# Optimization experiments

Hardware: AMD Instinct MI355X
Metric: run time of the kernel (lower is better)

## Reference

```python
import jax, jax.numpy as jnp
import numpy as np

M = 8192   # predicted boxes
N = 8192   # ground-truth boxes
W_CENTER, W_SIZE, W_IOU = 1.0, 0.5, 2.0
MATCH_THRESH = 5.0


def setup_inputs() -> dict:
    key = jax.random.key(0)
    k1, k2, k3, k4 = jax.random.split(key, 4)
    centers = jax.random.uniform(k1, (N, 3), dtype=jnp.float32) * 100.0
    sizes = jax.random.uniform(k2, (N, 3), dtype=jnp.float32) * 3.0 + 1.0
    yaw = jax.random.uniform(k3, (N, 1), dtype=jnp.float32) * (2.0 * jnp.pi) - jnp.pi
    gt_boxes = jnp.concatenate([centers, sizes, yaw], axis=1)  # [N,7]
    # preds = perturbed gts so the 5.0 m matching gate actually fires
    pred_boxes = gt_boxes + 0.5 * jax.random.normal(k4, (M, 7), dtype=jnp.float32)
    return {"pred_boxes": pred_boxes, "gt_boxes": gt_boxes}


def _greedy_match(pred_boxes, gt_boxes):
    """Sequential greedy nearest-center matching (torch loop -> lax.scan).
    Column deletion in the original is equivalent to masking with an
    availability vector: argmin over remaining columns with first-tie wins.
    Returns (mask [M] bool: pred i matched, idx [M] int: matched gt index)."""
    # [M,N] center distance matrix (the memory-heavy irregular part)
    diff = pred_boxes[:, None, :3] - gt_boxes[None, :, :3]
    dist = jnp.sqrt(jnp.sum(diff * diff, axis=-1))

    def step(avail, d_row):
        dm = jnp.where(avail, d_row, jnp.inf)
        j = jnp.argmin(dm)
        ok = dm[j] < MATCH_THRESH
        avail = avail.at[j].set(jnp.logical_and(avail[j], jnp.logical_not(ok)))
        return avail, (ok, j)

    avail0 = jnp.ones((gt_boxes.shape[0],), dtype=bool)
    _, (mask, idx) = jax.lax.scan(step, avail0, dist)
    return mask, idx


def _smooth_l1(x):
    a = jnp.abs(x)
    return jnp.where(a < 1.0, 0.5 * a * a, a - 0.5)


def _iou_2d(b1, b2):
    # axis-aligned BEV IoU using (x, y, l, w)
    x1, y1, l1, w1 = b1[:, 0], b1[:, 1], b1[:, 3], b1[:, 4]
    x2, y2, l2, w2 = b2[:, 0], b2[:, 1], b2[:, 3], b2[:, 4]
    iw = jnp.clip(jnp.minimum(x1 + l1 / 2, x2 + l2 / 2) - jnp.maximum(x1 - l1 / 2, x2 - l2 / 2), 0.0)
    ih = jnp.clip(jnp.minimum(y1 + w1 / 2, y2 + w2 / 2) - jnp.maximum(y1 - w1 / 2, y2 - w2 / 2), 0.0)
    inter = iw * ih
    union = l1 * w1 + l2 * w2 - inter
    return inter / (union + 1e-6)


def _loss(pred_boxes, gt_boxes, mask, idx):
    mg = gt_boxes[idx]                              # [M,7] matched gts
    m = mask.astype(pred_boxes.dtype)               # [M]
    k = jnp.maximum(jnp.sum(m), 1.0)                # number of matches
    loss_center = jnp.sum(m[:, None] * _smooth_l1(pred_boxes[:, :3] - mg[:, :3])) / (3.0 * k)
    loss_size = jnp.sum(m[:, None] * _smooth_l1(pred_boxes[:, 3:6] - mg[:, 3:6])) / (3.0 * k)
    d = pred_boxes[:, 6] - mg[:, 6]
    d = jnp.arctan2(jnp.sin(d), jnp.cos(d))         # wrap to (-pi, pi]
    loss_orient = jnp.sum(m * _smooth_l1(d)) / k
    loss_iou = jnp.sum(m * (1.0 - _iou_2d(pred_boxes, mg))) / k
    return W_CENTER * loss_center + W_SIZE * (loss_size + loss_orient) + W_IOU * loss_iou


def reference(pred_boxes, gt_boxes):
    mask, idx = _greedy_match(pred_boxes, gt_boxes)
    return _loss(pred_boxes, gt_boxes, mask, idx)
```

## Files before the change

### kernel.cpp

```cpp
#include <hip/hip_runtime.h>
#include <stdint.h>

#define MROWS 8192
#define NGT   8192
#define KC    8
#define KL    2
#define RPL   4
#define THRESH2_BITS 0x41C7FFFFu

__device__ __forceinline__ unsigned dist2_bits(float px, float py, float pz,
                                               float gx, float gy, float gz) {
#pragma clang fp contract(off)
  float dx = px - gx;
  float dy = py - gy;
  float dz = pz - gz;
  float s = (dx * dx + dy * dy) + dz * dz;
  return __float_as_uint(s);
}

__device__ __forceinline__ unsigned long long wave_min64(unsigned long long v) {
#pragma unroll
  for (int off = 32; off >= 1; off >>= 1) {
    unsigned long long o = __shfl_xor(v, off, 64);
    v = (o < v) ? o : v;
  }
  return v;
}

template <int K>
__device__ __forceinline__ void insert_sorted(unsigned (&kd)[K], unsigned (&ki)[K],
                                              unsigned key, unsigned j) {
#pragma unroll
  for (int t = K - 1; t >= 1; --t) {
    bool a = key < kd[t];
    bool b = key < kd[t - 1];
    if (a) {
      if (b) { kd[t] = kd[t - 1]; ki[t] = ki[t - 1]; }
      else   { kd[t] = key;       ki[t] = j; }
    }
  }
  if (key < kd[0]) { kd[0] = key; ki[0] = j; }
}

template <int K>
__device__ __forceinline__ void extract8(unsigned (&kd)[K], unsigned (&ki)[K], int lane,
                                         unsigned& resd, unsigned& resi,
                                         unsigned long long& e8) {
#pragma unroll
  for (int rr = 0; rr < KC; ++rr) {
    unsigned long long head = ((unsigned long long)kd[0] << 32) | (unsigned long long)ki[0];
    unsigned long long m = wave_min64(head);
    if (head == m) {
#pragma unroll
      for (int t = 0; t < K - 1; ++t) { kd[t] = kd[t + 1]; ki[t] = ki[t + 1]; }
      kd[K - 1] = 0xFFFFFFFFu; ki[K - 1] = 0xFFFFFFFFu;
    }
    if (lane == rr) { resd = (unsigned)(m >> 32); resi = (unsigned)m; }
    e8 = m;
  }
}

__global__ __launch_bounds__(256) void pack_kernel(const float* __restrict__ gt,
                                                   float4* __restrict__ cen) {
  int j = blockIdx.x * 256 + threadIdx.x;
  if (j < NGT) cen[j] = make_float4(gt[j * 7 + 0], gt[j * 7 + 1], gt[j * 7 + 2], 0.0f);
}

__global__ __launch_bounds__(256, 8) void topk_kernel(const float* __restrict__ pred,
                                                      const float4* __restrict__ cen,
                                                      unsigned* __restrict__ cand) {
  const int tid = threadIdx.x;
  const int lane = tid & 63;
  const int row = (blockIdx.x * 256 + tid) >> 6;

  float px = pred[(size_t)row * 7 + 0];
  float py = pred[(size_t)row * 7 + 1];
  float pz = pred[(size_t)row * 7 + 2];

  unsigned kd[KL], ki[KL];
#pragma unroll
  for (int t = 0; t < KL; ++t) { kd[t] = 0xFFFFFFFFu; ki[t] = 0xFFFFFFFFu; }

#pragma unroll 2
  for (int j0 = 0; j0 < NGT / 64; ++j0) {
    int j = j0 * 64 + lane;
    float4 c = cen[j];
    unsigned key = dist2_bits(px, py, pz, c.x, c.y, c.z);
    if (key < kd[KL - 1]) insert_sorted<KL>(kd, ki, key, (unsigned)j);
  }

  unsigned long long guard =
      ((unsigned long long)kd[KL - 1] << 32) | (unsigned long long)ki[KL - 1];
  unsigned resd = 0, resi = 0;
  unsigned long long e8 = 0;
  extract8<KL>(kd, ki, lane, resd, resi, e8);

  if (__ballot(guard < e8) != 0ull) {
    unsigned fd[KC], fi[KC];
#pragma unroll
    for (int t = 0; t < KC; ++t) { fd[t] = 0xFFFFFFFFu; fi[t] = 0xFFFFFFFFu; }
    for (int j0 = 0; j0 < NGT / 64; ++j0) {
      int j = j0 * 64 + lane;
      float4 c = cen[j];
      unsigned key = dist2_bits(px, py, pz, c.x, c.y, c.z);
      if (key < fd[KC - 1]) insert_sorted<KC>(fd, fi, key, (unsigned)j);
    }
    unsigned long long dummy;
    extract8<KC>(fd, fi, lane, resd, resi, dummy);
  }
  if (lane < KC)
    cand[(size_t)row * KC + lane] = (resi << 1) | (resd < THRESH2_BITS ? 1u : 0u);
}

__global__ __launch_bounds__(64) void greedy_kernel(const unsigned* __restrict__ cand,
                                                    const float* __restrict__ pred,
                                                    const float4* __restrict__ cen,
                                                    unsigned* __restrict__ match) {
  __shared__ unsigned avail[NGT / 32];
  __shared__ unsigned claim[NGT];
  const int lane = threadIdx.x;

  for (int w = lane; w < NGT / 32; w += 64) avail[w] = 0xFFFFFFFFu;
  for (int j = lane; j < NGT; j += 64) claim[j] = 0xFFFFFFFFu;
  __syncthreads();

  unsigned ci_[RPL][KC], ni_[RPL][KC];
  bool first = true;

  for (int base = 0; base < MROWS; base += 64 * RPL) {
    const int nAct = 64 * RPL;

    if (first) {
#pragma unroll
      for (int q = 0; q < RPL; ++q) {
        const uint4* cr = (const uint4*)(cand + (size_t)(base + lane + 64 * q) * KC);
        uint4 a = cr[0], b = cr[1];
        ci_[q][0] = a.x; ci_[q][1] = a.y; ci_[q][2] = a.z; ci_[q][3] = a.w;
        ci_[q][4] = b.x; ci_[q][5] = b.y; ci_[q][6] = b.z; ci_[q][7] = b.w;
      }
      first = false;
    } else {
#pragma unroll
      for (int q = 0; q < RPL; ++q)
#pragma unroll
        for (int t = 0; t < KC; ++t) ci_[q][t] = ni_[q][t];
    }
#pragma unroll
    for (int q = 0; q < RPL; ++q) {
      int pr = base + nAct + lane + 64 * q;
      if (pr >= MROWS) pr = MROWS - 1;
      const uint4* cr = (const uint4*)(cand + (size_t)pr * KC);
      uint4 a = cr[0], b = cr[1];
      ni_[q][0] = a.x; ni_[q][1] = a.y; ni_[q][2] = a.z; ni_[q][3] = a.w;
      ni_[q][4] = b.x; ni_[q][5] = b.y; ni_[q][6] = b.z; ni_[q][7] = b.w;
    }

    unsigned m[RPL];
#pragma unroll
    for (int q = 0; q < RPL; ++q) {
      unsigned mm = 0;
#pragma unroll
      for (int t = 0; t < KC; ++t) {
        unsigned g = ci_[q][t] >> 1;
        mm |= ((avail[g >> 5] >> (g & 31)) & 1u) << t;
      }
      m[q] = mm;
    }

    int floor_ = 0;
    unsigned pe[RPL];
    bool cl[RPL];
    int rounds = 0;

    while (true) {
      while (true) {
#pragma unroll
        for (int q = 0; q < RPL; ++q) {
          int o = lane + 64 * q;
          unsigned e = 0;
#pragma unroll
          for (int t = KC - 1; t >= 0; --t)
            if (m[q] & (1u << t)) e = ci_[q][t];
          pe[q] = e;
          cl[q] = (o >= floor_) && (m[q] != 0u) && (e & 1u);
        }
#pragma unroll
        for (int q = 0; q < RPL; ++q)
          if (cl[q]) atomicMin(&claim[pe[q] >> 1], (unsigned)(lane + 64 * q));
        __builtin_amdgcn_wave_barrier();
        bool any = false;
        bool lost[RPL];
#pragma unroll
        for (int q = 0; q < RPL; ++q) {
          lost[q] = cl[q] && (claim[pe[q] >> 1] < (unsigned)(lane + 64 * q));
          any |= lost[q];
        }
        if (__ballot(any) == 0ull) break;
#pragma unroll
        for (int q = 0; q < RPL; ++q)
          if (lost[q]) m[q] &= (m[q] - 1u);
        if (++rounds > 2100) {
#pragma unroll
          for (int q = 0; q < RPL; ++q)
            if (lane + 64 * q >= floor_) m[q] = 0u;
        }
      }

      unsigned fe = 0xFFFFu;
#pragma unroll
      for (int q = 0; q < RPL; ++q) {
        unsigned o = (unsigned)(lane + 64 * q);
        if (o >= (unsigned)floor_ && m[q] == 0u && o < fe) fe = o;
      }
#pragma unroll
      for (int off = 32; off >= 1; off >>= 1) {
        unsigned o2 = __shfl_xor(fe, off, 64);
        fe = o2 < fe ? o2 : fe;
      }
      int feI = (fe == 0xFFFFu) ? nAct : (int)fe;

#pragma unroll
      for (int q = 0; q < RPL; ++q) {
        int o = lane + 64 * q;
        if (o >= floor_ && o < feI) {
          unsigned g = pe[q] >> 1;
          match[base + o] = (cl[q] ? 0x80000000u : 0u) | g;
          if (cl[q]) atomicAnd(&avail[g >> 5], ~(1u << (g & 31)));
        }
      }
      __builtin_amdgcn_wave_barrier();
      if (feI == nAct) break;

      {
        const int r = base + feI;
        float fx = pred[(size_t)r * 7 + 0];
        float fy = pred[(size_t)r * 7 + 1];
        float fz = pred[(size_t)r * 7 + 2];
        unsigned long long best = ~0ull;
        for (int j0 = 0; j0 < NGT / 64; ++j0) {
          int j = j0 * 64 + lane;
          if ((avail[j >> 5] >> (j & 31)) & 1u) {
            float4 c = cen[j];
            unsigned sb = dist2_bits(fx, fy, fz, c.x, c.y, c.z);
            unsigned long long key = ((unsigned long long)sb << 32) | (unsigned)j;
            if (key < best) best = key;
          }
        }
        unsigned long long mm2 = wave_min64(best);
        unsigned gstar = 0xFFFFFFFFu;
        if (mm2 != ~0ull) {
          unsigned sb = (unsigned)(mm2 >> 32);
          unsigned j = (unsigned)mm2;
          bool ok = sb < THRESH2_BITS;
          if (lane == 0) {
            match[r] = (ok ? 0x80000000u : 0u) | j;
            if (ok) atomicAnd(&avail[j >> 5], ~(1u << (j & 31)));
          }
          if (ok) gstar = j;
        } else if (lane == 0) {
          match[r] = 0u;
        }
        __builtin_amdgcn_wave_barrier();
        if (gstar != 0xFFFFFFFFu) {
#pragma unroll
          for (int q = 0; q < RPL; ++q)
#pragma unroll
            for (int t = 0; t < KC; ++t)
              if ((ci_[q][t] >> 1) == gstar) m[q] &= ~(1u << t);
        }
        floor_ = feI + 1;
        if (floor_ >= nAct) break;
      }
    }

#pragma unroll
    for (int q = 0; q < RPL; ++q)
#pragma unroll
      for (int t = 0; t < KC; ++t) claim[ci_[q][t] >> 1] = 0xFFFFFFFFu;
    __builtin_amdgcn_wave_barrier();
  }
}

__device__ __forceinline__ float smooth_l1(float x) {
  float a = fabsf(x);
  return (a < 1.0f) ? (0.5f * a * a) : (a - 0.5f);
}

__global__ __launch_bounds__(256) void loss_kernel(const float* __restrict__ pred,
                                                   const float* __restrict__ gt,
                                                   const unsigned* __restrict__ match,
                                                   float* __restrict__ acc) {
  int i = blockIdx.x * 256 + threadIdx.x;
  float vc = 0.f, vs = 0.f, vo = 0.f, vi = 0.f, vk = 0.f;
  if (i < MROWS) {
    unsigned r = match[i];
    if (r & 0x80000000u) {
      unsigned j = r & 0x7FFFFFFFu;
      float p[7], g[7];
#pragma unroll
      for (int t = 0; t < 7; ++t) { p[t] = pred[i * 7 + t]; g[t] = gt[j * 7 + t]; }
      vc = smooth_l1(p[0] - g[0]) + smooth_l1(p[1] - g[1]) + smooth_l1(p[2] - g[2]);
      vs = smooth_l1(p[3] - g[3]) + smooth_l1(p[4] - g[4]) + smooth_l1(p[5] - g[5]);
      float d = p[6] - g[6];
      float w = d - 6.283185307179586f * rintf(d * 0.15915494309189535f);
      vo = smooth_l1(w);
      float iw = fminf(p[0] + p[3] * 0.5f, g[0] + g[3] * 0.5f) -
                 fmaxf(p[0] - p[3] * 0.5f, g[0] - g[3] * 0.5f);
      iw = fmaxf(iw, 0.0f);
      float ih = fminf(p[1] + p[4] * 0.5f, g[1] + g[4] * 0.5f) -
                 fmaxf(p[1] - p[4] * 0.5f, g[1] - g[4] * 0.5f);
      ih = fmaxf(ih, 0.0f);
      float inter = iw * ih;
      float uni = p[3] * p[4] + g[3] * g[4] - inter;
      vi = 1.0f - inter / (uni + 1e-6f);
      vk = 1.0f;
    }
  }
#pragma unroll
  for (int off = 32; off >= 1; off >>= 1) {
    vc += __shfl_down(vc, off, 64);
    vs += __shfl_down(vs, off, 64);
    vo += __shfl_down(vo, off, 64);
    vi += __shfl_down(vi, off, 64);
    vk += __shfl_down(vk, off, 64);
  }
  if ((threadIdx.x & 63) == 0) {
    atomicAdd(&acc[0], vc);
    atomicAdd(&acc[1], vs);
    atomicAdd(&acc[2], vo);
    atomicAdd(&acc[3], vi);
    atomicAdd(&acc[4], vk);
  }
}

__global__ void finalize_kernel(const float* __restrict__ acc, float* __restrict__ out) {
  float k = fmaxf(acc[4], 1.0f);
  float loss = acc[0] / (3.0f * k)
             + 0.5f * (acc[1] / (3.0f * k) + acc[2] / k)
             + 2.0f * (acc[3] / k);
  out[0] = loss;
}

extern "C" void kernel_launch(void* const* d_in, const int* in_sizes, int n_in,
                              void* d_out, int out_size, void* d_ws, size_t ws_size,
                              hipStream_t stream) {
  const float* pred = (const float*)d_in[0];
  const float* gt   = (const float*)d_in[1];
  char* ws = (char*)d_ws;
  float* acc       = (float*)ws;
  unsigned* match  = (unsigned*)(ws + 1024);
  unsigned* cand   = (unsigned*)(ws + 33792);
  float4* cen      = (float4*)(ws + 295936);

  hipMemsetAsync(acc, 0, 32, stream);
  pack_kernel<<<NGT / 256, 256, 0, stream>>>(gt, cen);
  topk_kernel<<<MROWS / 4, 256, 0, stream>>>(pred, cen, cand);
  greedy_kernel<<<1, 64, 0, stream>>>(cand, pred, cen, match);
  loss_kernel<<<MROWS / 256, 256, 0, stream>>>(pred, gt, match, acc);
  finalize_kernel<<<1, 1, 0, stream>>>(acc, (float*)d_out);
}
```

Baseline: 258.1 us.

## Tile GT centers through shared memory, two rows per wave; fold finalize into loss

The top-k distance kernel now stages GT centers through a double-buffered shared-memory tile and has each wave process two prediction rows. Each loaded center is reused across rows, which halves global/L2 traffic per row and the number of blocks. The finalize kernel is removed: the last loss block, found with an atomic ticket counter, computes the output, saving one launch. The trade-offs are added block barriers, more registers (launch bounds relaxed to 4), and fewer waves in flight.

```diff
diff --git a/kernel.cpp b/kernel.cpp
--- a/kernel.cpp
+++ b/kernel.cpp
@@ -5,6 +5,7 @@
 #define NGT   8192
 #define KC    8
 #define KL    2
+#define RPW   2
 #define RPL   4
 #define THRESH2_BITS 0x41C7FFFFu
 
@@ -66,50 +67,78 @@
   if (j < NGT) cen[j] = make_float4(gt[j * 7 + 0], gt[j * 7 + 1], gt[j * 7 + 2], 0.0f);
 }
 
-__global__ __launch_bounds__(256, 8) void topk_kernel(const float* __restrict__ pred,
+__global__ __launch_bounds__(256, 4) void topk_kernel(const float* __restrict__ pred,
                                                       const float4* __restrict__ cen,
                                                       unsigned* __restrict__ cand) {
+  __shared__ float4 tile[2][256];
   const int tid = threadIdx.x;
   const int lane = tid & 63;
-  const int row = (blockIdx.x * 256 + tid) >> 6;
-
-  float px = pred[(size_t)row * 7 + 0];
-  float py = pred[(size_t)row * 7 + 1];
-  float pz = pred[(size_t)row * 7 + 2];
-
-  unsigned kd[KL], ki[KL];
-#pragma unroll
-  for (int t = 0; t < KL; ++t) { kd[t] = 0xFFFFFFFFu; ki[t] = 0xFFFFFFFFu; }
-
-#pragma unroll 2
-  for (int j0 = 0; j0 < NGT / 64; ++j0) {
-    int j = j0 * 64 + lane;
-    float4 c = cen[j];
-    unsigned key = dist2_bits(px, py, pz, c.x, c.y, c.z);
-    if (key < kd[KL - 1]) insert_sorted<KL>(kd, ki, key, (unsigned)j);
-  }
-
-  unsigned long long guard =
-      ((unsigned long long)kd[KL - 1] << 32) | (unsigned long long)ki[KL - 1];
-  unsigned resd = 0, resi = 0;
-  unsigned long long e8 = 0;
-  extract8<KL>(kd, ki, lane, resd, resi, e8);
-
-  if (__ballot(guard < e8) != 0ull) {
-    unsigned fd[KC], fi[KC];
-#pragma unroll
-    for (int t = 0; t < KC; ++t) { fd[t] = 0xFFFFFFFFu; fi[t] = 0xFFFFFFFFu; }
-    for (int j0 = 0; j0 < NGT / 64; ++j0) {
-      int j = j0 * 64 + lane;
-      float4 c = cen[j];
-      unsigned key = dist2_bits(px, py, pz, c.x, c.y, c.z);
-      if (key < fd[KC - 1]) insert_sorted<KC>(fd, fi, key, (unsigned)j);
-    }
-    unsigned long long dummy;
-    extract8<KC>(fd, fi, lane, resd, resi, dummy);
-  }
-  if (lane < KC)
-    cand[(size_t)row * KC + lane] = (resi << 1) | (resd < THRESH2_BITS ? 1u : 0u);
+  const int wave = (blockIdx.x * 256 + tid) >> 6;
+  const int r0 = wave * RPW;
+
+  float px[RPW], py[RPW], pz[RPW];
+#pragma unroll
+  for (int r = 0; r < RPW; ++r) {
+    px[r] = pred[(size_t)(r0 + r) * 7 + 0];
+    py[r] = pred[(size_t)(r0 + r) * 7 + 1];
+    pz[r] = pred[(size_t)(r0 + r) * 7 + 2];
+  }
+
+  unsigned kd[RPW][KL], ki[RPW][KL];
+#pragma unroll
+  for (int r = 0; r < RPW; ++r)
+#pragma unroll
+    for (int t = 0; t < KL; ++t) { kd[r][t] = 0xFFFFFFFFu; ki[r][t] = 0xFFFFFFFFu; }
+
+  tile[0][tid] = cen[tid];
+  __syncthreads();
+
+  for (int t = 0; t < NGT / 256; ++t) {
+    float4 nreg;
+    if (t < NGT / 256 - 1) nreg = cen[(t + 1) * 256 + tid];
+
+#pragma unroll
+    for (int i = 0; i < 4; ++i) {
+      float4 c = tile[t & 1][i * 64 + lane];
+      int j = t * 256 + i * 64 + lane;
+#pragma unroll
+      for (int r = 0; r < RPW; ++r) {
+        unsigned key = dist2_bits(px[r], py[r], pz[r], c.x, c.y, c.z);
+        if (key < kd[r][KL - 1]) insert_sorted<KL>(kd[r], ki[r], key, (unsigned)j);
+      }
+    }
+    __syncthreads();
+    if (t < NGT / 256 - 1) {
+      tile[(t + 1) & 1][tid] = nreg;
+      __syncthreads();
+    }
+  }
+
+#pragma unroll
+  for (int r = 0; r < RPW; ++r) {
+    const int row = r0 + r;
+    unsigned long long guard =
+        ((unsigned long long)kd[r][KL - 1] << 32) | (unsigned long long)ki[r][KL - 1];
+    unsigned resd = 0, resi = 0;
+    unsigned long long e8 = 0;
+    extract8<KL>(kd[r], ki[r], lane, resd, resi, e8);
+
+    if (__ballot(guard < e8) != 0ull) {
+      unsigned fd[KC], fi[KC];
+#pragma unroll
+      for (int t = 0; t < KC; ++t) { fd[t] = 0xFFFFFFFFu; fi[t] = 0xFFFFFFFFu; }
+      for (int j0 = 0; j0 < NGT / 64; ++j0) {
+        int j = j0 * 64 + lane;
+        float4 c = cen[j];
+        unsigned key = dist2_bits(px[r], py[r], pz[r], c.x, c.y, c.z);
+        if (key < fd[KC - 1]) insert_sorted<KC>(fd, fi, key, (unsigned)j);
+      }
+      unsigned long long dummy;
+      extract8<KC>(fd, fi, lane, resd, resi, dummy);
+    }
+    if (lane < KC)
+      cand[(size_t)row * KC + lane] = (resi << 1) | (resd < THRESH2_BITS ? 1u : 0u);
+  }
 }
 
 __global__ __launch_bounds__(64) void greedy_kernel(const unsigned* __restrict__ cand,
@@ -289,7 +318,8 @@
 __global__ __launch_bounds__(256) void loss_kernel(const float* __restrict__ pred,
                                                    const float* __restrict__ gt,
                                                    const unsigned* __restrict__ match,
-                                                   float* __restrict__ acc) {
+                                                   float* __restrict__ acc,
+                                                   float* __restrict__ out) {
   int i = blockIdx.x * 256 + threadIdx.x;
   float vc = 0.f, vs = 0.f, vo = 0.f, vi = 0.f, vk = 0.f;
   if (i < MROWS) {
@@ -331,14 +361,20 @@
     atomicAdd(&acc[3], vi);
     atomicAdd(&acc[4], vk);
   }
-}
-
-__global__ void finalize_kernel(const float* __restrict__ acc, float* __restrict__ out) {
-  float k = fmaxf(acc[4], 1.0f);
-  float loss = acc[0] / (3.0f * k)
-             + 0.5f * (acc[1] / (3.0f * k) + acc[2] / k)
-             + 2.0f * (acc[3] / k);
-  out[0] = loss;
+  __syncthreads();
+  if (threadIdx.x == 0) {
+    __threadfence();
+    unsigned t = atomicAdd((unsigned*)&acc[6], 1u);
+    if (t == gridDim.x - 1) {
+      float a0 = atomicAdd(&acc[0], 0.0f);
+      float a1 = atomicAdd(&acc[1], 0.0f);
+      float a2 = atomicAdd(&acc[2], 0.0f);
+      float a3 = atomicAdd(&acc[3], 0.0f);
+      float a4 = atomicAdd(&acc[4], 0.0f);
+      float k = fmaxf(a4, 1.0f);
+      out[0] = a0 / (3.0f * k) + 0.5f * (a1 / (3.0f * k) + a2 / k) + 2.0f * (a3 / k);
+    }
+  }
 }
 
 extern "C" void kernel_launch(void* const* d_in, const int* in_sizes, int n_in,
@@ -352,10 +388,9 @@
   unsigned* cand   = (unsigned*)(ws + 33792);
   float4* cen      = (float4*)(ws + 295936);
 
-  hipMemsetAsync(acc, 0, 32, stream);
+  hipMemsetAsync(acc, 0, 64, stream);
   pack_kernel<<<NGT / 256, 256, 0, stream>>>(gt, cen);
-  topk_kernel<<<MROWS / 4, 256, 0, stream>>>(pred, cen, cand);
+  topk_kernel<<<MROWS / (RPW * 4), 256, 0, stream>>>(pred, cen, cand);
   greedy_kernel<<<1, 64, 0, stream>>>(cand, pred, cen, match);
-  loss_kernel<<<MROWS / 256, 256, 0, stream>>>(pred, gt, match, acc);
-  finalize_kernel<<<1, 1, 0, stream>>>(acc, (float*)d_out);
-}
+  loss_kernel<<<MROWS / 256, 256, 0, stream>>>(pred, gt, match, acc, (float*)d_out);
+}
```

After: 278.1 us. +7.7%, slower.
